# Performance work log

Measured on AMD Instinct MI355X. Metric: run time of the kernel, lower is better.

## Reference

```python
import jax, jax.numpy as jnp
import numpy as np

N, D_IN, WID, LAT, DPD, H, N_SEG = 131072, 128, 512, 512, 128, 8, 256


def cumulative_segment_mean(data, segment_ids):
    # prefix mean that resets at each new (sorted) segment id
    n = data.shape[0]
    idx = jnp.arange(n)
    seg_start = jnp.concatenate([jnp.ones((1,), bool), segment_ids[1:] != segment_ids[:-1]])
    # index of the first element of each token's segment
    start_idx = jax.lax.associative_scan(jnp.maximum, jnp.where(seg_start, idx, 0))
    cs = jnp.cumsum(data, axis=0)
    base = jnp.where((start_idx > 0)[:, None], cs[jnp.maximum(start_idx - 1, 0)], jnp.zeros((), data.dtype))
    count = (idx - start_idx + 1).astype(data.dtype)[:, None]
    return (cs - base) / count


def setup_inputs() -> dict:
    key = jax.random.key(0)
    ks = jax.random.split(key, 12)
    he = lambda k, sh: jax.random.normal(k, sh, jnp.float32) * np.sqrt(2.0 / sh[0]).astype(np.float32)
    inputs = jax.random.normal(ks[0], (N, D_IN), jnp.float32)
    segment_ids = jnp.sort(jax.random.randint(ks[1], (N,), 0, N_SEG, dtype=jnp.int64))
    return {
        "inputs": inputs,
        "segment_ids": segment_ids,
        "W1": he(ks[2], (D_IN, WID)), "b1": jnp.zeros((WID,), jnp.float32),
        "W2": he(ks[3], (WID, WID)), "b2": jnp.zeros((WID,), jnp.float32),
        "W3": he(ks[4], (WID, LAT)), "b3": jnp.zeros((LAT,), jnp.float32),
        "Wr": he(ks[5], (LAT, LAT)), "br": jnp.zeros((LAT,), jnp.float32),
        "W_k": he(ks[6], (LAT + D_IN, DPD * H)),
        "W_q": jax.random.normal(ks[7], (H, DPD), jnp.float32) * 0.05,
    }


def reference(inputs, segment_ids, W1, b1, W2, b2, W3, b3, Wr, br, W_k, W_q):
    relu = jax.nn.relu
    h = relu(inputs @ W1 + b1)          # psi layer 1
    h = relu(h @ W2 + b2)               # psi layer 2
    encoded = relu(h @ W3 + b3)         # psi latent projection
    agg = cumulative_segment_mean(encoded, segment_ids)
    agg = relu(agg @ Wr + br)           # rho
    combined = jnp.concatenate([inputs, agg], axis=-1)   # [N, D_IN+LAT]
    keys = (combined @ W_k).reshape(inputs.shape[0], H, DPD)  # split+stack heads
    preattn = jnp.einsum('nhd,hd->nh', keys, W_q) / jnp.sqrt(jnp.float32(DPD))
    return preattn
```

## Files before the change

kernel.cpp:

```cpp
#include <hip/hip_runtime.h>
#include <hip/hip_bf16.h>
#include <stdint.h>

typedef unsigned short ushortT;
typedef __bf16 bf16x8 __attribute__((ext_vector_type(8)));
typedef float f32x4 __attribute__((ext_vector_type(4)));

#define N_TOK 131072
#define NSEG  256
#define RSPL  8

__device__ __forceinline__ uint32_t f2bf(float f) {
  union { float f; uint32_t u; } c; c.f = f;
  uint32_t u = c.u;
  u += 0x7fffu + ((u >> 16) & 1u);
  return u >> 16;
}
__device__ __forceinline__ float bf2f(uint32_t b) {
  union { uint32_t u; float f; } c; c.u = b << 16;
  return c.f;
}

__device__ __forceinline__ void gload_lds16(const void* g, void* l) {
  __builtin_amdgcn_global_load_lds(
      (const __attribute__((address_space(1))) void*)g,
      (__attribute__((address_space(3))) void*)l, 16, 0, 0);
}


__global__ void transpose_bf16_kernel(const float* __restrict__ W, ushortT* __restrict__ WT,
                                      int Kd, int Nd) {
  int i = blockIdx.x * 256 + threadIdx.x;
  if (i < Kd * Nd) {
    int n = i / Kd, k = i % Kd;
    WT[i] = (ushortT)f2bf(W[(size_t)k * Nd + n]);
  }
}

__global__ void weff_kernel(const float* __restrict__ Wk, const float* __restrict__ Wq,
                            ushortT* __restrict__ weffT) {
  const int c = blockIdx.x;
  const int lane = threadIdx.x;
  const float rs = 0.08838834764831845f;
#pragma unroll
  for (int h = 0; h < 8; ++h) {
    float acc = Wk[(size_t)c * 1024 + h * 128 + lane] * Wq[h * 128 + lane]
              + Wk[(size_t)c * 1024 + h * 128 + 64 + lane] * Wq[h * 128 + 64 + lane];
#pragma unroll
    for (int off = 32; off >= 1; off >>= 1) acc += __shfl_xor(acc, off, 64);
    if (lane == 0) {
      weffT[h * 640 + c]       = (ushortT)f2bf(acc * rs);
      weffT[(h + 8) * 640 + c] = 0;
    }
  }
}

__global__ void seg_bounds_kernel(const int* __restrict__ seg, int* __restrict__ gbnd) {
  const int s = (int)threadIdx.x + (int)blockIdx.x * 512;
  if (s > NSEG) return;
  int lo = 0, hi = N_TOK;
  while (lo < hi) { int m = (lo + hi) >> 1; if (seg[m] < s) lo = m + 1; else hi = m; }
  gbnd[s] = lo;
}


template <int K, bool RELU, bool BIAS, bool XF32>
__global__ __launch_bounds__(256, 3)
void gemm_m97_kernel(const void* __restrict__ Av, const ushortT* __restrict__ BT,
                     const float* __restrict__ bias, ushortT* __restrict__ C) {
  __shared__ ushortT lA[128 * 64];
  __shared__ ushortT lB[128 * 64];
  constexpr int NT = K / 64;

  const int nwg  = (int)gridDim.x;
  const int cpx  = nwg >> 3;
  const int flat = (int)blockIdx.x;
  const int swz  = (flat & 7) * cpx + (flat >> 3);
  const int bm   = swz >> 2;
  const int bn   = swz & 3;

  const int t = (int)threadIdx.x;
  const int w = t >> 6, lane = t & 63;
  const int wm = w >> 1, wn = w & 1;
  const int q = lane >> 4, lr = lane & 15;

  const int srow = t >> 3;
  const int slc  = (t & 7) ^ (srow & 7);

  const ushortT* Ab = nullptr;
  const float*   Xf = nullptr;
  if (XF32) Xf = (const float*)Av + (size_t)(bm * 128 + srow) * 128 + slc * 8;
  else      Ab = (const ushortT*)Av + (size_t)(bm * 128 + srow) * K + slc * 8;
  const ushortT* Bg = BT + (size_t)(bn * 128 + srow) * K + slc * 8;

  f32x4 acc[4][4];
#pragma unroll
  for (int i = 0; i < 4; ++i)
#pragma unroll
    for (int j = 0; j < 4; ++j) acc[i][j] = 0.f;

  const int cc0 = (q ^ (lr & 7)) << 4;
  const int cc1 = ((4 + q) ^ (lr & 7)) << 4;
  const char* lAc = (const char*)lA;
  const char* lBc = (const char*)lB;

#pragma unroll 1
  for (int kt = 0; kt < NT; ++kt) {
    {
      const ushortT* src = Bg + kt * 64;
#pragma unroll
      for (int j = 0; j < 4; ++j)
        gload_lds16(src + (size_t)j * 32 * K, (char*)lB + j * 4096 + t * 16);
    }
    if (XF32) {
      const float* src = Xf + kt * 64;
#pragma unroll
      for (int j = 0; j < 4; ++j) {
        const float4 v0 = *(const float4*)(src + (size_t)j * 32 * 128);
        const float4 v1 = *(const float4*)(src + (size_t)j * 32 * 128 + 4);
        uint4 pk;
        pk.x = f2bf(v0.x) | (f2bf(v0.y) << 16);
        pk.y = f2bf(v0.z) | (f2bf(v0.w) << 16);
        pk.z = f2bf(v1.x) | (f2bf(v1.y) << 16);
        pk.w = f2bf(v1.z) | (f2bf(v1.w) << 16);
        *(uint4*)((char*)lA + j * 4096 + t * 16) = pk;
      }
    } else {
      const ushortT* src = Ab + kt * 64;
#pragma unroll
      for (int j = 0; j < 4; ++j)
        gload_lds16(src + (size_t)j * 32 * K, (char*)lA + j * 4096 + t * 16);
    }
    __syncthreads();

    bf16x8 a0[4], a1[4], b0[4], b1[4];
#pragma unroll
    for (int m = 0; m < 4; ++m) {
      const int ro = (wm * 64 + m * 16 + lr) * 128;
      a0[m] = *(const bf16x8*)(lAc + ro + cc0);
      a1[m] = *(const bf16x8*)(lAc + ro + cc1);
    }
#pragma unroll
    for (int n = 0; n < 4; ++n) {
      const int ro = (wn * 64 + n * 16 + lr) * 128;
      b0[n] = *(const bf16x8*)(lBc + ro + cc0);
      b1[n] = *(const bf16x8*)(lBc + ro + cc1);
    }

    __builtin_amdgcn_s_setprio(1);
#pragma unroll
    for (int n = 0; n < 4; ++n)
#pragma unroll
      for (int m = 0; m < 4; ++m)
        acc[m][n] = __builtin_amdgcn_mfma_f32_16x16x32_bf16(a0[m], b0[n], acc[m][n], 0, 0, 0);
#pragma unroll
    for (int n = 0; n < 4; ++n)
#pragma unroll
      for (int m = 0; m < 4; ++m)
        acc[m][n] = __builtin_amdgcn_mfma_f32_16x16x32_bf16(a1[m], b1[n], acc[m][n], 0, 0, 0);
    __builtin_amdgcn_s_setprio(0);

    __syncthreads();
  }

  const int row0 = bm * 128 + wm * 64 + q * 4;
  const int col0 = bn * 128 + wn * 64 + lr;
#pragma unroll
  for (int n = 0; n < 4; ++n) {
    const int col = col0 + n * 16;
    const float bvv = BIAS ? bias[col] : 0.f;
#pragma unroll
    for (int m = 0; m < 4; ++m) {
#pragma unroll
      for (int r = 0; r < 4; ++r) {
        float v = acc[m][n][r] + bvv;
        if (RELU) v = fmaxf(v, 0.f);
        C[(size_t)(row0 + m * 16 + r) * 512 + col] = (ushortT)f2bf(v);
      }
    }
  }
}


__global__ __launch_bounds__(256)
void seg_sum_kernel(const ushortT* __restrict__ z, const int* __restrict__ gbnd,
                    float* __restrict__ part, int c0, int rows) {
  const int s  = (int)blockIdx.x >> 3;
  const int rg = (int)blockIdx.x & 7;
  const int t  = (int)threadIdx.x;

  const int gb0 = gbnd[s], gb1 = gbnd[s + 1];
  int beg = gb0 > c0 ? gb0 : c0;
  int end = gb1 < c0 + rows ? gb1 : c0 + rows;
  int len = end - beg; if (len < 0) len = 0;
  const int r0 = beg + ((len * rg) >> 3);
  const int r1 = beg + ((len * (rg + 1)) >> 3);

  float a0 = 0.f, a1 = 0.f;
  const uint32_t* __restrict__ zp = (const uint32_t*)z;
  int r = r0;
  for (; r + 8 <= r1; r += 8) {
    uint32_t v[8];
#pragma unroll
    for (int i = 0; i < 8; ++i) v[i] = zp[(size_t)(r + i - c0) * 256 + t];
#pragma unroll
    for (int i = 0; i < 8; ++i) { a0 += bf2f(v[i] & 0xffffu); a1 += bf2f(v[i] >> 16); }
  }
  for (; r < r1; ++r) {
    const uint32_t v = zp[(size_t)(r - c0) * 256 + t];
    a0 += bf2f(v & 0xffffu); a1 += bf2f(v >> 16);
  }
  float2 pv; pv.x = a0; pv.y = a1;
  ((float2*)part)[(s * 8 + rg) * 256 + t] = pv;
}

__global__ __launch_bounds__(256)
void seg_scan2_kernel(const ushortT* __restrict__ z, ushortT* __restrict__ gout,
                      const int* __restrict__ gbnd, const float* __restrict__ br,
                      const float* __restrict__ part,
                      const float* __restrict__ cin, float* __restrict__ cout,
                      int c0, int rows) {
  const int s  = (int)blockIdx.x >> 3;
  const int rg = (int)blockIdx.x & 7;
  const int t  = (int)threadIdx.x;

  const int gb0 = gbnd[s], gb1 = gbnd[s + 1];
  int beg = gb0 > c0 ? gb0 : c0;
  int end = gb1 < c0 + rows ? gb1 : c0 + rows;
  int len = end - beg; if (len < 0) len = 0;
  const int r0 = beg + ((len * rg) >> 3);
  const int r1 = beg + ((len * (rg + 1)) >> 3);

  const float2 cv = ((const float2*)cin)[s * 256 + t];
  float a0 = cv.x, a1 = cv.y;
  for (int q2 = 0; q2 < rg; ++q2) {
    const float2 pv = ((const float2*)part)[(s * 8 + q2) * 256 + t];
    a0 += pv.x; a1 += pv.y;
  }
  int cb = c0 - gb0; if (cb < 0) cb = 0;
  const int seglen = gb1 - gb0; if (cb > seglen) cb = seglen;
  const int cnt0 = cb + (r0 - beg);

  const float b0 = br[2 * t], b1v = br[2 * t + 1];
  const uint32_t* __restrict__ zp = (const uint32_t*)z;
  uint32_t* __restrict__ gp = (uint32_t*)gout;

  int r = r0;
  for (; r + 8 <= r1; r += 8) {
    uint32_t v[8];
#pragma unroll
    for (int i = 0; i < 8; ++i) v[i] = zp[(size_t)(r + i - c0) * 256 + t];
#pragma unroll
    for (int i = 0; i < 8; ++i) {
      a0 += bf2f(v[i] & 0xffffu);
      a1 += bf2f(v[i] >> 16);
      const float inv = 1.0f / (float)(cnt0 + (r + i) - r0 + 1);
      const float g0 = fmaxf(fmaf(a0, inv, b0), 0.f);
      const float g1 = fmaxf(fmaf(a1, inv, b1v), 0.f);
      gp[(size_t)(r + i - c0) * 256 + t] = f2bf(g0) | (f2bf(g1) << 16);
    }
  }
  for (; r < r1; ++r) {
    const uint32_t v = zp[(size_t)(r - c0) * 256 + t];
    a0 += bf2f(v & 0xffffu);
    a1 += bf2f(v >> 16);
    const float inv = 1.0f / (float)(cnt0 + r - r0 + 1);
    const float g0 = fmaxf(fmaf(a0, inv, b0), 0.f);
    const float g1 = fmaxf(fmaf(a1, inv, b1v), 0.f);
    gp[(size_t)(r - c0) * 256 + t] = f2bf(g0) | (f2bf(g1) << 16);
  }

  if (rg == 7) {
    float2 co; co.x = a0; co.y = a1;
    ((float2*)cout)[s * 256 + t] = co;
  }
}


__global__ __launch_bounds__(256)
void final_mfma_kernel(const float* __restrict__ X, const ushortT* __restrict__ g,
                       const ushortT* __restrict__ weffT, float* __restrict__ out) {
  __shared__ char lw[16 * 1296];
  const int t = (int)threadIdx.x;

#pragma unroll
  for (int i = 0; i < 5; ++i) {
    const int idx = i * 256 + t;
    const int row = idx / 80, c = idx % 80;
    *(uint4*)(lw + row * 1296 + c * 16) =
        *(const uint4*)((const char*)weffT + row * 1280 + c * 16);
  }
  __syncthreads();

  const int wv = t >> 6, lane = t & 63;
  const int q = lane >> 4, lr = lane & 15;
  const int rbase = (int)blockIdx.x * 128 + wv * 32;

  f32x4 acc[2];
  acc[0] = 0.f; acc[1] = 0.f;

#pragma unroll
  for (int kk = 0; kk < 20; ++kk) {
    const bf16x8 b = *(const bf16x8*)(lw + lr * 1296 + kk * 64 + q * 16);
#pragma unroll
    for (int mt = 0; mt < 2; ++mt) {
      const int row = rbase + mt * 16 + lr;
      union { ushortT u[8]; bf16x8 v; } a;
      if (kk < 4) {
        const float* xr = X + (size_t)row * 128 + kk * 32 + q * 8;
        const float4 v0 = *(const float4*)xr;
        const float4 v1 = *(const float4*)(xr + 4);
        a.u[0] = (ushortT)f2bf(v0.x); a.u[1] = (ushortT)f2bf(v0.y);
        a.u[2] = (ushortT)f2bf(v0.z); a.u[3] = (ushortT)f2bf(v0.w);
        a.u[4] = (ushortT)f2bf(v1.x); a.u[5] = (ushortT)f2bf(v1.y);
        a.u[6] = (ushortT)f2bf(v1.z); a.u[7] = (ushortT)f2bf(v1.w);
      } else {
        a.v = *(const bf16x8*)(g + (size_t)row * 512 + (kk - 4) * 32 + q * 8);
      }
      acc[mt] = __builtin_amdgcn_mfma_f32_16x16x32_bf16(a.v, b, acc[mt], 0, 0, 0);
    }
  }

  if (lr < 8) {
#pragma unroll
    for (int mt = 0; mt < 2; ++mt)
#pragma unroll
      for (int r = 0; r < 4; ++r)
        out[(size_t)(rbase + mt * 16 + q * 4 + r) * 8 + lr] = acc[mt][r];
  }
}


extern "C" void kernel_launch(void* const* d_in, const int* in_sizes, int n_in,
                              void* d_out, int out_size, void* d_ws, size_t ws_size,
                              hipStream_t stream) {
  const float* X  = (const float*)d_in[0];
  const int*   sg = (const int*)d_in[1];
  const float* W1 = (const float*)d_in[2];
  const float* b1 = (const float*)d_in[3];
  const float* W2 = (const float*)d_in[4];
  const float* b2 = (const float*)d_in[5];
  const float* W3 = (const float*)d_in[6];
  const float* b3 = (const float*)d_in[7];
  const float* Wr = (const float*)d_in[8];
  const float* br = (const float*)d_in[9];
  const float* Wk = (const float*)d_in[10];
  const float* Wq = (const float*)d_in[11];
  float* out = (float*)d_out;

  const size_t szW1T  = 512 * 128 * 2;
  const size_t szWT   = 512 * 512 * 2;
  const size_t szWeff = 16 * 640 * 2;
  const size_t szPart = (size_t)NSEG * RSPL * 256 * 2 * 4;
  const size_t szCar  = (size_t)NSEG * 256 * 2 * 4;
  const size_t szBnd  = (NSEG + 1) * 4;
  const size_t fixed  = szW1T + 3 * szWT + szWeff + szPart + 2 * szCar + szBnd + 512;

  int CH = 0;
  const int cands[6] = {131072, 65536, 32768, 16384, 8192, 4096};
  for (int i = 0; i < 6; ++i) {
    const size_t need = fixed + 2 * (size_t)cands[i] * 512 * 2;
    if (need <= ws_size) { CH = cands[i]; break; }
  }
  if (CH == 0) CH = 4096;

  char* p = (char*)d_ws;
  ushortT* W1T   = (ushortT*)p; p += szW1T;
  ushortT* W2T   = (ushortT*)p; p += szWT;
  ushortT* W3T   = (ushortT*)p; p += szWT;
  ushortT* WrT   = (ushortT*)p; p += szWT;
  ushortT* weffT = (ushortT*)p; p += szWeff;
  float*   part  = (float*)p;   p += szPart;
  float*   carA  = (float*)p;   p += szCar;
  float*   carB  = (float*)p;   p += szCar;
  int*     gbnd  = (int*)p;     p += (szBnd + 255) & ~255ull;
  ushortT* p1    = (ushortT*)p; p += (size_t)CH * 512 * 2;
  ushortT* p2    = (ushortT*)p;

  transpose_bf16_kernel<<<(512 * 128 + 255) / 256, 256, 0, stream>>>(W1, W1T, 128, 512);
  transpose_bf16_kernel<<<(512 * 512 + 255) / 256, 256, 0, stream>>>(W2, W2T, 512, 512);
  transpose_bf16_kernel<<<(512 * 512 + 255) / 256, 256, 0, stream>>>(W3, W3T, 512, 512);
  transpose_bf16_kernel<<<(512 * 512 + 255) / 256, 256, 0, stream>>>(Wr, WrT, 512, 512);
  weff_kernel<<<640, 64, 0, stream>>>(Wk, Wq, weffT);
  seg_bounds_kernel<<<1, 512, 0, stream>>>(sg, gbnd);
  hipMemsetAsync(carA, 0, szCar, stream);

  int par = 0;
  for (int c0 = 0; c0 < N_TOK; c0 += CH) {
    const int gG = (CH / 128) * 4;
    float* cin  = par ? carB : carA;
    float* cout = par ? carA : carB;
    gemm_m97_kernel<128, true,  true,  true ><<<gG, 256, 0, stream>>>(X + (size_t)c0 * 128, W1T, b1, p1);
    gemm_m97_kernel<512, true,  true,  false><<<gG, 256, 0, stream>>>(p1, W2T, b2, p2);
    gemm_m97_kernel<512, true,  true,  false><<<gG, 256, 0, stream>>>(p2, W3T, b3, p1);
    gemm_m97_kernel<512, false, false, false><<<gG, 256, 0, stream>>>(p1, WrT, nullptr, p2);
    seg_sum_kernel <<<NSEG * RSPL, 256, 0, stream>>>(p2, gbnd, part, c0, CH);
    seg_scan2_kernel<<<NSEG * RSPL, 256, 0, stream>>>(p2, p1, gbnd, br, part,
                                                      cin, cout, c0, CH);
    final_mfma_kernel<<<CH / 128, 256, 0, stream>>>(X + (size_t)c0 * 128, p1, weffT,
                                                    out + (size_t)c0 * 8);
    par ^= 1;
  }
}
```

Measured before the change: 433.0 us.

## Fuse input-part of final projection into first GEMM and raise occupancy hint

```diff
diff --git a/kernel.cpp b/kernel.cpp
--- a/kernel.cpp
+++ b/kernel.cpp
@@ -64,10 +64,11 @@
 }
 
 
-template <int K, bool RELU, bool BIAS, bool XF32>
-__global__ __launch_bounds__(256, 3)
+template <int K, bool RELU, bool BIAS, bool XF32, bool OUTP>
+__global__ __launch_bounds__(256, 4)
 void gemm_m97_kernel(const void* __restrict__ Av, const ushortT* __restrict__ BT,
-                     const float* __restrict__ bias, ushortT* __restrict__ C) {
+                     const float* __restrict__ bias, ushortT* __restrict__ C,
+                     const ushortT* __restrict__ weffT, float* __restrict__ outp) {
   __shared__ ushortT lA[128 * 64];
   __shared__ ushortT lB[128 * 64];
   constexpr int NT = K / 64;
@@ -98,6 +99,17 @@
   for (int i = 0; i < 4; ++i)
 #pragma unroll
     for (int j = 0; j < 4; ++j) acc[i][j] = 0.f;
+
+  f32x4 acc_out[2];
+  bf16x8 wxf[2][2];
+  if (OUTP) {
+    acc_out[0] = 0.f; acc_out[1] = 0.f;
+#pragma unroll
+    for (int kt = 0; kt < 2; ++kt)
+#pragma unroll
+      for (int kk = 0; kk < 2; ++kk)
+        wxf[kt][kk] = *(const bf16x8*)(weffT + lr * 640 + kt * 64 + kk * 32 + q * 8);
+  }
 
   const int cc0 = (q ^ (lr & 7)) << 4;
   const int cc1 = ((4 + q) ^ (lr & 7)) << 4;
@@ -160,7 +172,25 @@
         acc[m][n] = __builtin_amdgcn_mfma_f32_16x16x32_bf16(a1[m], b1[n], acc[m][n], 0, 0, 0);
     __builtin_amdgcn_s_setprio(0);
 
+    if (OUTP && bn == 0) {
+#pragma unroll
+      for (int mi = 0; mi < 2; ++mi) {
+        const int ro = (w * 32 + mi * 16 + lr) * 128;
+        const bf16x8 xa0 = *(const bf16x8*)(lAc + ro + cc0);
+        const bf16x8 xa1 = *(const bf16x8*)(lAc + ro + cc1);
+        acc_out[mi] = __builtin_amdgcn_mfma_f32_16x16x32_bf16(xa0, wxf[kt][0], acc_out[mi], 0, 0, 0);
+        acc_out[mi] = __builtin_amdgcn_mfma_f32_16x16x32_bf16(xa1, wxf[kt][1], acc_out[mi], 0, 0, 0);
+      }
+    }
     __syncthreads();
+  }
+
+  if (OUTP && bn == 0 && lr < 8) {
+#pragma unroll
+    for (int mi = 0; mi < 2; ++mi)
+#pragma unroll
+      for (int r = 0; r < 4; ++r)
+        outp[(size_t)(bm * 128 + w * 32 + mi * 16 + q * 4 + r) * 8 + lr] = acc_out[mi][r];
   }
 
   const int row0 = bm * 128 + wm * 64 + q * 4;
@@ -278,7 +308,7 @@
 
 
 __global__ __launch_bounds__(256)
-void final_mfma_kernel(const float* __restrict__ X, const ushortT* __restrict__ g,
+void final_mfma_kernel(const ushortT* __restrict__ g,
                        const ushortT* __restrict__ weffT, float* __restrict__ out) {
   __shared__ char lw[16 * 1296];
   const int t = (int)threadIdx.x;
@@ -298,26 +328,22 @@
 
   f32x4 acc[2];
   acc[0] = 0.f; acc[1] = 0.f;
-
-#pragma unroll
-  for (int kk = 0; kk < 20; ++kk) {
-    const bf16x8 b = *(const bf16x8*)(lw + lr * 1296 + kk * 64 + q * 16);
+  if (lr < 8) {
+#pragma unroll
+    for (int mt = 0; mt < 2; ++mt)
+#pragma unroll
+      for (int r = 0; r < 4; ++r)
+        acc[mt][r] = out[(size_t)(rbase + mt * 16 + q * 4 + r) * 8 + lr];
+  }
+
+#pragma unroll
+  for (int kk = 0; kk < 16; ++kk) {
+    const bf16x8 b = *(const bf16x8*)(lw + lr * 1296 + (kk + 4) * 64 + q * 16);
 #pragma unroll
     for (int mt = 0; mt < 2; ++mt) {
       const int row = rbase + mt * 16 + lr;
-      union { ushortT u[8]; bf16x8 v; } a;
-      if (kk < 4) {
-        const float* xr = X + (size_t)row * 128 + kk * 32 + q * 8;
-        const float4 v0 = *(const float4*)xr;
-        const float4 v1 = *(const float4*)(xr + 4);
-        a.u[0] = (ushortT)f2bf(v0.x); a.u[1] = (ushortT)f2bf(v0.y);
-        a.u[2] = (ushortT)f2bf(v0.z); a.u[3] = (ushortT)f2bf(v0.w);
-        a.u[4] = (ushortT)f2bf(v1.x); a.u[5] = (ushortT)f2bf(v1.y);
-        a.u[6] = (ushortT)f2bf(v1.z); a.u[7] = (ushortT)f2bf(v1.w);
-      } else {
-        a.v = *(const bf16x8*)(g + (size_t)row * 512 + (kk - 4) * 32 + q * 8);
-      }
-      acc[mt] = __builtin_amdgcn_mfma_f32_16x16x32_bf16(a.v, b, acc[mt], 0, 0, 0);
+      const bf16x8 a = *(const bf16x8*)(g + (size_t)row * 512 + kk * 32 + q * 8);
+      acc[mt] = __builtin_amdgcn_mfma_f32_16x16x32_bf16(a, b, acc[mt], 0, 0, 0);
     }
   }
 
@@ -390,15 +416,19 @@
     const int gG = (CH / 128) * 4;
     float* cin  = par ? carB : carA;
     float* cout = par ? carA : carB;
-    gemm_m97_kernel<128, true,  true,  true ><<<gG, 256, 0, stream>>>(X + (size_t)c0 * 128, W1T, b1, p1);
-    gemm_m97_kernel<512, true,  true,  false><<<gG, 256, 0, stream>>>(p1, W2T, b2, p2);
-    gemm_m97_kernel<512, true,  true,  false><<<gG, 256, 0, stream>>>(p2, W3T, b3, p1);
-    gemm_m97_kernel<512, false, false, false><<<gG, 256, 0, stream>>>(p1, WrT, nullptr, p2);
+    float* outc = out + (size_t)c0 * 8;
+    gemm_m97_kernel<128, true,  true,  true,  true ><<<gG, 256, 0, stream>>>(
+        X + (size_t)c0 * 128, W1T, b1, p1, weffT, outc);
+    gemm_m97_kernel<512, true,  true,  false, false><<<gG, 256, 0, stream>>>(
+        p1, W2T, b2, p2, nullptr, nullptr);
+    gemm_m97_kernel<512, true,  true,  false, false><<<gG, 256, 0, stream>>>(
+        p2, W3T, b3, p1, nullptr, nullptr);
+    gemm_m97_kernel<512, false, false, false, false><<<gG, 256, 0, stream>>>(
+        p1, WrT, nullptr, p2, nullptr, nullptr);
     seg_sum_kernel <<<NSEG * RSPL, 256, 0, stream>>>(p2, gbnd, part, c0, CH);
     seg_scan2_kernel<<<NSEG * RSPL, 256, 0, stream>>>(p2, p1, gbnd, br, part,
                                                       cin, cout, c0, CH);
-    final_mfma_kernel<<<CH / 128, 256, 0, stream>>>(X + (size_t)c0 * 128, p1, weffT,
-                                                    out + (size_t)c0 * 8);
+    final_mfma_kernel<<<CH / 128, 256, 0, stream>>>(p1, weffT, outc);
     par ^= 1;
   }
 }
```

New measurement: 639.0 us. +47.6%, slower.
